# Optimization experiments

Measured on AMD Instinct MI355X. Metric: run time of the kernel, lower is better.

The kernel has to match this reference:

```python
import jax, jax.numpy as jnp
import numpy as np

N, D_IN, F = 65536, 512, 256
E = 524288
BATCH, K1 = 32, 200
BN_EPS = 1e-5


def setup_inputs() -> dict:
    key = jax.random.key(0)
    ks = iter(jax.random.split(key, 64))

    def nrm(shape, s=0.05):
        return jax.random.normal(next(ks), shape, jnp.float32) * s

    inp = {
        "feat": jax.random.normal(next(ks), (N, D_IN), jnp.float32),
        "A": jax.random.randint(next(ks), (2, E), 0, N, dtype=jnp.int32),
        "h1id": jax.random.randint(next(ks), (BATCH * K1,), 0, N // BATCH, dtype=jnp.int32),
        "batch": BATCH,
    }
    dims = [(D_IN, F), (F, F), (F, F), (F, F)]
    for i, (di, do) in enumerate(dims, 1):
        inp[f"eps{i}"] = jnp.zeros((), jnp.float32)          # GINConv train_eps, init 0
        inp[f"w{i}a"] = nrm((di, do)); inp[f"b{i}a"] = jnp.zeros((do,), jnp.float32)
        inp[f"w{i}b"] = nrm((do, do)); inp[f"b{i}b"] = jnp.zeros((do,), jnp.float32)
        inp[f"g{i}"] = jnp.ones((do,), jnp.float32)          # BN gamma
        inp[f"be{i}"] = jnp.zeros((do,), jnp.float32)        # BN beta
        inp[f"m{i}"] = nrm((do,))                            # BN running mean
        inp[f"v{i}"] = jax.random.uniform(next(ks), (do,), jnp.float32, 0.5, 1.5)  # BN running var
    inp["wc1"] = nrm((F, F)); inp["bc1"] = jnp.zeros((F,), jnp.float32)
    inp["pa"] = jnp.full((F,), 0.25, jnp.float32)            # PReLU per-channel slope
    inp["wc2"] = nrm((F, 2)); inp["bc2"] = jnp.zeros((2,), jnp.float32)
    return inp


def _gin_conv(x, src, dst, eps, wa, ba, wb, bb, g, be, m, v):
    # sum aggregation over in-edges: aggr[i] = sum_{(j->i)} x[j]
    aggr = jax.ops.segment_sum(x[src], dst, num_segments=N)
    h = (1.0 + eps) * x + aggr
    h = jax.nn.relu(h @ wa + ba) @ wb + bb
    # BatchNorm1d in eval mode (running stats)
    return (h - m) * jax.lax.rsqrt(v + BN_EPS) * g + be


def _forward(feat, A, h1id, batch,
             eps1, w1a, b1a, w1b, b1b, g1, be1, m1, v1,
             eps2, w2a, b2a, w2b, b2b, g2, be2, m2, v2,
             eps3, w3a, b3a, w3b, b3b, g3, be3, m3, v3,
             eps4, w4a, b4a, w4b, b4b, g4, be4, m4, v4,
             wc1, bc1, pa, wc2, bc2):
    src, dst = A[0], A[1]
    h = jax.nn.relu(_gin_conv(feat, src, dst, eps1, w1a, b1a, w1b, b1b, g1, be1, m1, v1))
    h = jax.nn.relu(_gin_conv(h, src, dst, eps2, w2a, b2a, w2b, b2b, g2, be2, m2, v2))
    h = jax.nn.relu(_gin_conv(h, src, dst, eps3, w3a, b3a, w3b, b3b, g3, be3, m3, v3))
    h = _gin_conv(h, src, dst, eps4, w4a, b4a, w4b, b4b, g4, be4, m4, v4)
    score = h.reshape(batch, -1, F)                      # [B, n_per_graph, F]
    idx = h1id.reshape(batch, K1)
    edge_feat = jnp.take_along_axis(score, idx[:, :, None], axis=1)  # [B, K1, F]
    ef = edge_feat.reshape(-1, F)
    hc = ef @ wc1 + bc1
    hc = jnp.where(hc > 0, hc, pa * hc)                  # PReLU(256)
    return hc @ wc2 + bc2                                # [B*K1, 2]


def reference(feat, A, h1id, batch,
              eps1, w1a, b1a, w1b, b1b, g1, be1, m1, v1,
              eps2, w2a, b2a, w2b, b2b, g2, be2, m2, v2,
              eps3, w3a, b3a, w3b, b3b, g3, be3, m3, v3,
              eps4, w4a, b4a, w4b, b4b, g4, be4, m4, v4,
              wc1, bc1, pa, wc2, bc2):
    return _forward(feat, A, h1id, batch,
                    eps1, w1a, b1a, w1b, b1b, g1, be1, m1, v1,
                    eps2, w2a, b2a, w2b, b2b, g2, be2, m2, v2,
                    eps3, w3a, b3a, w3b, b3b, g3, be3, m3, v3,
                    eps4, w4a, b4a, w4b, b4b, g4, be4, m4, v4,
                    wc1, bc1, pa, wc2, bc2)
```

## Files before the change

kernel.cpp:

```cpp
#include <hip/hip_runtime.h>

typedef unsigned short u16;
typedef unsigned int   u32;
typedef __bf16  bf16x8 __attribute__((ext_vector_type(8)));
typedef float   f32x4  __attribute__((ext_vector_type(4)));
typedef u32     u32x4  __attribute__((ext_vector_type(4)));

#define NN 65536
#define NE 524288
#define FD 256

typedef const __attribute__((address_space(1))) void* gas_p;
typedef __attribute__((address_space(3))) void* las_p;
#define GLDS16(g, l) __builtin_amdgcn_global_load_lds((gas_p)(const void*)(g), (las_p)(void*)(l), 16, 0, 0)

__device__ __forceinline__ u16 f2bf(float f){
  u32 u = __float_as_uint(f);
  u += 0x7fffu + ((u >> 16) & 1u);
  return (u16)(u >> 16);
}
__device__ __forceinline__ float bf2f(u32 lo16){
  return __uint_as_float(lo16 << 16);
}
__device__ __forceinline__ void acc8(float* a, uint4 v){
  a[0] += bf2f(v.x & 0xffffu); a[1] += bf2f(v.x >> 16);
  a[2] += bf2f(v.y & 0xffffu); a[3] += bf2f(v.y >> 16);
  a[4] += bf2f(v.z & 0xffffu); a[5] += bf2f(v.z >> 16);
  a[6] += bf2f(v.w & 0xffffu); a[7] += bf2f(v.w >> 16);
}

__global__ __launch_bounds__(256) void prep_k(
    const float* __restrict__ w1a, const float* __restrict__ w1b,
    const float* __restrict__ w2a, const float* __restrict__ w2b,
    const float* __restrict__ w3a, const float* __restrict__ w3b,
    const float* __restrict__ w4a, const float* __restrict__ w4b,
    const float* __restrict__ wc1, u16* __restrict__ wT)
{
  int idx = blockIdx.x * 256 + threadIdx.x;
  const float* src; int base, K, local;
  if (idx < 131072){ src = w1a; base = 0; K = 512; local = idx; }
  else {
    local = idx - 131072;
    int j = local >> 16;
    local &= 65535;
    K = 256;
    base = 131072 + j * 65536;
    switch (j){
      case 0: src = w1b; break;
      case 1: src = w2a; break;
      case 2: src = w2b; break;
      case 3: src = w3a; break;
      case 4: src = w3b; break;
      case 5: src = w4a; break;
      case 6: src = w4b; break;
      default: src = wc1; break;
    }
  }
  int n = local & 255;
  int k = local >> 8;
  wT[base + n * K + k] = f2bf(src[k * 256 + n]);
}

__global__ __launch_bounds__(256) void hist_k(const int* __restrict__ dst, int* __restrict__ deg){
  int e = blockIdx.x * 256 + threadIdx.x;
  atomicAdd(&deg[dst[e]], 1);
}

__global__ __launch_bounds__(1024) void scan_k(const int* __restrict__ deg, int* __restrict__ rs){
  __shared__ int part[1024];
  int t = threadIdx.x;
  int base = t * 64;
  int sum = 0;
  for (int i = 0; i < 64; ++i) sum += deg[base + i];
  part[t] = sum;
  __syncthreads();
  for (int off = 1; off < 1024; off <<= 1){
    int v = 0;
    if (t >= off) v = part[t - off];
    __syncthreads();
    part[t] += v;
    __syncthreads();
  }
  int run = part[t] - sum;
  for (int i = 0; i < 64; ++i){ rs[base + i] = run; run += deg[base + i]; }
  if (t == 1023) rs[65536] = part[1023];
}

__global__ __launch_bounds__(256) void scat_k(
    const int* __restrict__ src, const int* __restrict__ dst,
    const int* __restrict__ rs, int* __restrict__ cursor, int* __restrict__ csr)
{
  int e = blockIdx.x * 256 + threadIdx.x;
  int d = dst[e];
  int pos = atomicAdd(&cursor[d], 1);
  csr[rs[d] + pos] = src[e];
}

template<int AF32, int MODE, int RELU, int K>
__global__ __launch_bounds__(512) void gemm_k(
    const void* __restrict__ Ap, const u16* __restrict__ Bt,
    u16* __restrict__ C,
    const float* __restrict__ p0, const float* __restrict__ p1,
    const float* __restrict__ p2, const float* __restrict__ p3,
    const float* __restrict__ p4)
{
  __shared__ u16 lds[32768];
  u16* As = lds;
  u16* Bs = lds + 8192;
  const int t    = threadIdx.x;
  const int lane = t & 63;
  const int w    = t >> 6;
  const int wm   = w & 1;
  const int wn   = w >> 1;
  const int m0   = blockIdx.x * 128;
  const int mrow = lane & 15;
  const int quad = lane >> 4;

  f32x4 acc[4][4];
  const f32x4 zero = {0.f, 0.f, 0.f, 0.f};
  #pragma unroll
  for (int i = 0; i < 4; ++i)
    #pragma unroll
    for (int j = 0; j < 4; ++j) acc[i][j] = zero;

  const u16* Ab = (const u16*)Ap;
  const float* Af = (const float*)Ap;

  for (int k0 = 0; k0 < K; k0 += 64){
    if (AF32){
      #pragma unroll
      for (int i = 0; i < 2; ++i){
        int p   = i * 512 + t;
        int row = p >> 3;
        const float* s = Af + (size_t)(m0 + row) * K + k0 + (p & 7) * 8;
        float4 x0 = *(const float4*)s;
        float4 x1 = *(const float4*)(s + 4);
        union { u32x4 q; u16 h[8]; } u;
        u.h[0] = f2bf(x0.x); u.h[1] = f2bf(x0.y); u.h[2] = f2bf(x0.z); u.h[3] = f2bf(x0.w);
        u.h[4] = f2bf(x1.x); u.h[5] = f2bf(x1.y); u.h[6] = f2bf(x1.z); u.h[7] = f2bf(x1.w);
        int dst = (p & ~7) | ((p & 7) ^ (row & 7));
        *(u32x4*)&As[dst * 8] = u.q;
      }
    } else {
      #pragma unroll
      for (int i = 0; i < 2; ++i){
        int p   = i * 512 + t;
        int row = p >> 3;
        int ch  = (p & 7) ^ (row & 7);
        GLDS16(Ab + (size_t)(m0 + row) * K + k0 + ch * 8, &As[p * 8]);
      }
    }
    #pragma unroll
    for (int i = 0; i < 4; ++i){
      int p   = i * 512 + t;
      int row = p >> 3;
      int ch  = (p & 7) ^ (row & 7);
      GLDS16(Bt + (size_t)row * K + k0 + ch * 8, &Bs[p * 8]);
    }
    __syncthreads();
    #pragma unroll
    for (int ks = 0; ks < 2; ++ks){
      bf16x8 af[4], bq[4];
      #pragma unroll
      for (int mi = 0; mi < 4; ++mi){
        int r  = wm * 64 + mi * 16 + mrow;
        int ch = (quad + ks * 4) ^ (r & 7);
        af[mi] = *(const bf16x8*)&As[(r * 8 + ch) * 8];
      }
      #pragma unroll
      for (int ni = 0; ni < 4; ++ni){
        int rb = wn * 64 + ni * 16 + mrow;
        int ch = (quad + ks * 4) ^ (rb & 7);
        bq[ni] = *(const bf16x8*)&Bs[(rb * 8 + ch) * 8];
      }
      #pragma unroll
      for (int mi = 0; mi < 4; ++mi)
        #pragma unroll
        for (int ni = 0; ni < 4; ++ni)
          acc[mi][ni] = __builtin_amdgcn_mfma_f32_16x16x32_bf16(af[mi], bq[ni], acc[mi][ni], 0, 0, 0);
    }
    __syncthreads();
  }

  #pragma unroll
  for (int ni = 0; ni < 4; ++ni){
    int c  = wn * 64 + ni * 16 + mrow;
    float scale = 1.f, shift = 0.f, slope = 0.f;
    if (MODE == 1){
      float s = p0[c] * rsqrtf(p3[c] + 1e-5f);
      scale = s;
      shift = (p4[c] - p2[c]) * s + p1[c];
    }
    if (MODE == 2){ shift = p0[c]; slope = p1[c]; }
    #pragma unroll
    for (int mi = 0; mi < 4; ++mi){
      int rbase = wm * 64 + mi * 16 + quad * 4;
      #pragma unroll
      for (int reg = 0; reg < 4; ++reg){
        float v = acc[mi][ni][reg];
        if (MODE == 1){
          v = v * scale + shift;
          if (RELU) v = fmaxf(v, 0.f);
        }
        if (MODE == 2){
          v += shift;
          v = v > 0.f ? v : slope * v;
        }
        lds[(rbase + reg) * 256 + c] = f2bf(v);
      }
    }
  }
  __syncthreads();
  #pragma unroll
  for (int i = 0; i < 8; ++i){
    int p  = i * 512 + t;
    int r  = p >> 5;
    int ch = p & 31;
    u32x4 q = *(const u32x4*)&lds[r * 256 + ch * 8];
    *(u32x4*)&C[(size_t)(m0 + r) * 256 + ch * 8] = q;
  }
}

template<int GATH>
__global__ __launch_bounds__(256) void agg_k(
    const u16* __restrict__ y, const int* __restrict__ rs, const int* __restrict__ csr,
    const float* __restrict__ epsp, const float* __restrict__ bias,
    const int* __restrict__ gidx, u16* __restrict__ tout)
{
  int sub    = threadIdx.x >> 5;
  int lane32 = threadIdx.x & 31;
  int idx    = blockIdx.x * 8 + sub;
  int node;
  if (GATH) node = (idx / 200) * 2048 + gidx[idx];
  else      node = idx;
  int f0 = lane32 * 8;
  float e1 = 1.0f + epsp[0];
  int s0 = rs[node], s1 = rs[node + 1];
  float a[8] = {0.f,0.f,0.f,0.f,0.f,0.f,0.f,0.f};
  int e = s0;
  for (; e + 4 <= s1; e += 4){
    int sa = csr[e], sb = csr[e+1], sc = csr[e+2], sd = csr[e+3];
    uint4 va = *(const uint4*)(y + (size_t)sa * 256 + f0);
    uint4 vb = *(const uint4*)(y + (size_t)sb * 256 + f0);
    uint4 vc = *(const uint4*)(y + (size_t)sc * 256 + f0);
    uint4 vd = *(const uint4*)(y + (size_t)sd * 256 + f0);
    acc8(a, va); acc8(a, vb); acc8(a, vc); acc8(a, vd);
  }
  for (; e < s1; ++e){
    int s = csr[e];
    acc8(a, *(const uint4*)(y + (size_t)s * 256 + f0));
  }
  uint4 own = *(const uint4*)(y + (size_t)node * 256 + f0);
  float ow[8];
  ow[0] = bf2f(own.x & 0xffffu); ow[1] = bf2f(own.x >> 16);
  ow[2] = bf2f(own.y & 0xffffu); ow[3] = bf2f(own.y >> 16);
  ow[4] = bf2f(own.z & 0xffffu); ow[5] = bf2f(own.z >> 16);
  ow[6] = bf2f(own.w & 0xffffu); ow[7] = bf2f(own.w >> 16);
  float4 b0 = *(const float4*)(bias + f0);
  float4 b1 = *(const float4*)(bias + f0 + 4);
  float r[8];
  r[0] = fmaxf(e1 * ow[0] + a[0] + b0.x, 0.f);
  r[1] = fmaxf(e1 * ow[1] + a[1] + b0.y, 0.f);
  r[2] = fmaxf(e1 * ow[2] + a[2] + b0.z, 0.f);
  r[3] = fmaxf(e1 * ow[3] + a[3] + b0.w, 0.f);
  r[4] = fmaxf(e1 * ow[4] + a[4] + b1.x, 0.f);
  r[5] = fmaxf(e1 * ow[5] + a[5] + b1.y, 0.f);
  r[6] = fmaxf(e1 * ow[6] + a[6] + b1.z, 0.f);
  r[7] = fmaxf(e1 * ow[7] + a[7] + b1.w, 0.f);
  uint4 o;
  o.x = (u32)f2bf(r[0]) | ((u32)f2bf(r[1]) << 16);
  o.y = (u32)f2bf(r[2]) | ((u32)f2bf(r[3]) << 16);
  o.z = (u32)f2bf(r[4]) | ((u32)f2bf(r[5]) << 16);
  o.w = (u32)f2bf(r[6]) | ((u32)f2bf(r[7]) << 16);
  *(uint4*)(tout + (size_t)idx * 256 + f0) = o;
}

__global__ __launch_bounds__(256) void head_k(
    const u16* __restrict__ hc, const float* __restrict__ wc2,
    const float* __restrict__ bc2, float* __restrict__ out)
{
  int row  = blockIdx.x * 4 + (threadIdx.x >> 6);
  int lane = threadIdx.x & 63;
  int f0   = lane * 4;
  uint2 hv = *(const uint2*)(hc + (size_t)row * 256 + f0);
  float h0 = bf2f(hv.x & 0xffffu), h1 = bf2f(hv.x >> 16);
  float h2 = bf2f(hv.y & 0xffffu), h3 = bf2f(hv.y >> 16);
  float4 wa = *(const float4*)(wc2 + f0 * 2);
  float4 wb = *(const float4*)(wc2 + f0 * 2 + 4);
  float acc0 = h0 * wa.x + h1 * wa.z + h2 * wb.x + h3 * wb.z;
  float acc1 = h0 * wa.y + h1 * wa.w + h2 * wb.y + h3 * wb.w;
  #pragma unroll
  for (int off = 32; off > 0; off >>= 1){
    acc0 += __shfl_xor(acc0, off);
    acc1 += __shfl_xor(acc1, off);
  }
  if (lane == 0){
    out[row * 2]     = acc0 + bc2[0];
    out[row * 2 + 1] = acc1 + bc2[1];
  }
}

extern "C" void kernel_launch(void* const* d_in, const int* in_sizes, int n_in,
                              void* d_out, int out_size, void* d_ws, size_t ws_size,
                              hipStream_t stream)
{
  const float* feat = (const float*)d_in[0];
  const int*   A    = (const int*)d_in[1];
  const int*   h1id = (const int*)d_in[2];
  const float* eps[4] = {(const float*)d_in[4],  (const float*)d_in[13], (const float*)d_in[22], (const float*)d_in[31]};
  const float* wa [4] = {(const float*)d_in[5],  (const float*)d_in[14], (const float*)d_in[23], (const float*)d_in[32]};
  const float* ba [4] = {(const float*)d_in[6],  (const float*)d_in[15], (const float*)d_in[24], (const float*)d_in[33]};
  const float* wb [4] = {(const float*)d_in[7],  (const float*)d_in[16], (const float*)d_in[25], (const float*)d_in[34]};
  const float* bb [4] = {(const float*)d_in[8],  (const float*)d_in[17], (const float*)d_in[26], (const float*)d_in[35]};
  const float* g  [4] = {(const float*)d_in[9],  (const float*)d_in[18], (const float*)d_in[27], (const float*)d_in[36]};
  const float* be [4] = {(const float*)d_in[10], (const float*)d_in[19], (const float*)d_in[28], (const float*)d_in[37]};
  const float* m  [4] = {(const float*)d_in[11], (const float*)d_in[20], (const float*)d_in[29], (const float*)d_in[38]};
  const float* v  [4] = {(const float*)d_in[12], (const float*)d_in[21], (const float*)d_in[30], (const float*)d_in[39]};
  const float* wc1 = (const float*)d_in[40];
  const float* bc1 = (const float*)d_in[41];
  const float* pa  = (const float*)d_in[42];
  const float* wc2 = (const float*)d_in[43];
  const float* bc2 = (const float*)d_in[44];

  char* ws = (char*)d_ws;
  u16* wT     = (u16*)(ws + 0);
  int* deg    = (int*)(ws + 1310720);
  int* rs     = (int*)(ws + 1572864);
  int* cursor = (int*)(ws + 1835264);
  int* csr    = (int*)(ws + 2097408);
  u16* ybuf   = (u16*)(ws + 4194560);
  u16* tbuf   = (u16*)(ws + 37748992);
  u16* hbuf   = (u16*)(ws + 71303424);
  u16* h4     = (u16*)(ws + 104857856);
  u16* hc     = (u16*)(ws + 108134656);

  u16* w1aT = wT;
  u16* w1bT = wT + 131072;
  u16* w2aT = wT + 196608;
  u16* w2bT = wT + 262144;
  u16* w3aT = wT + 327680;
  u16* w3bT = wT + 393216;
  u16* w4aT = wT + 458752;
  u16* w4bT = wT + 524288;
  u16* wc1T = wT + 589824;

  hipMemsetAsync(deg, 0, 65536 * 4, stream);
  hipMemsetAsync(cursor, 0, 65536 * 4, stream);
  prep_k<<<2560, 256, 0, stream>>>(wa[0], wb[0], wa[1], wb[1], wa[2], wb[2], wa[3], wb[3], wc1, wT);
  hist_k<<<NE / 256, 256, 0, stream>>>(A + NE, deg);
  scan_k<<<1, 1024, 0, stream>>>(deg, rs);
  scat_k<<<NE / 256, 256, 0, stream>>>(A, A + NE, rs, cursor, csr);

  const u16* waT[4] = {w1aT, w2aT, w3aT, w4aT};
  const u16* wbT[4] = {w1bT, w2bT, w3bT, w4bT};

  gemm_k<1,0,0,512><<<512, 512, 0, stream>>>(feat, waT[0], ybuf,
      nullptr, nullptr, nullptr, nullptr, nullptr);
  agg_k<0><<<NN / 8, 256, 0, stream>>>(ybuf, rs, csr, eps[0], ba[0], nullptr, tbuf);
  gemm_k<0,1,1,256><<<512, 512, 0, stream>>>(tbuf, wbT[0], hbuf,
      g[0], be[0], m[0], v[0], bb[0]);

  for (int l = 1; l <= 2; ++l){
    gemm_k<0,0,0,256><<<512, 512, 0, stream>>>(hbuf, waT[l], ybuf,
        nullptr, nullptr, nullptr, nullptr, nullptr);
    agg_k<0><<<NN / 8, 256, 0, stream>>>(ybuf, rs, csr, eps[l], ba[l], nullptr, tbuf);
    gemm_k<0,1,1,256><<<512, 512, 0, stream>>>(tbuf, wbT[l], hbuf,
        g[l], be[l], m[l], v[l], bb[l]);
  }

  gemm_k<0,0,0,256><<<512, 512, 0, stream>>>(hbuf, waT[3], ybuf,
      nullptr, nullptr, nullptr, nullptr, nullptr);
  agg_k<1><<<800, 256, 0, stream>>>(ybuf, rs, csr, eps[3], ba[3], h1id, tbuf);
  gemm_k<0,1,0,256><<<50, 512, 0, stream>>>(tbuf, wbT[3], h4,
      g[3], be[3], m[3], v[3], bb[3]);

  gemm_k<0,2,0,256><<<50, 512, 0, stream>>>(h4, wc1T, hc,
      bc1, pa, nullptr, nullptr, nullptr);
  head_k<<<1600, 256, 0, stream>>>(hc, wc2, bc2, (float*)d_out);

  (void)in_sizes; (void)n_in; (void)out_size; (void)ws_size;
}
```

Before: 628.6 us.

## Double-buffer GEMM LDS staging with smaller tiles and pre-convert features to bf16

The GEMM kernel now uses 64-row tiles, 256 threads and K-steps of 32. It double-buffers the A and B tiles in LDS, issuing the next global_load_lds batch before computing the current one and using explicit vmcnt waits and barriers. Input features are converted to bf16 by a separate conv_k kernel, so the first GEMM no longer converts fp32 inline. The smaller tiles double the grid size, which raises occupancy, but each B tile is now reloaded by twice as many blocks and the conversion adds an extra pass over the feature matrix.

```diff
diff --git a/kernel.cpp b/kernel.cpp
--- a/kernel.cpp
+++ b/kernel.cpp
@@ -14,6 +14,10 @@
 typedef __attribute__((address_space(3))) void* las_p;
 #define GLDS16(g, l) __builtin_amdgcn_global_load_lds((gas_p)(const void*)(g), (las_p)(void*)(l), 16, 0, 0)
 
+#define PIPE_BARRIER()  asm volatile("s_barrier" ::: "memory")
+#define PIPE_WAIT5()    asm volatile("s_waitcnt vmcnt(5)" ::: "memory")
+#define PIPE_WAIT0()    asm volatile("s_waitcnt vmcnt(0)" ::: "memory")
+
 __device__ __forceinline__ u16 f2bf(float f){
   u32 u = __float_as_uint(f);
   u += 0x7fffu + ((u >> 16) & 1u);
@@ -27,6 +31,16 @@
   a[2] += bf2f(v.y & 0xffffu); a[3] += bf2f(v.y >> 16);
   a[4] += bf2f(v.z & 0xffffu); a[5] += bf2f(v.z >> 16);
   a[6] += bf2f(v.w & 0xffffu); a[7] += bf2f(v.w >> 16);
+}
+
+__global__ __launch_bounds__(256) void conv_k(const float* __restrict__ src, u16* __restrict__ dst){
+  int idx = blockIdx.x * 256 + threadIdx.x;
+  const float4* s = (const float4*)(src + (size_t)idx * 8);
+  float4 x0 = s[0], x1 = s[1];
+  union { u32x4 q; u16 h[8]; } u;
+  u.h[0] = f2bf(x0.x); u.h[1] = f2bf(x0.y); u.h[2] = f2bf(x0.z); u.h[3] = f2bf(x0.w);
+  u.h[4] = f2bf(x1.x); u.h[5] = f2bf(x1.y); u.h[6] = f2bf(x1.z); u.h[7] = f2bf(x1.w);
+  *(u32x4*)(dst + (size_t)idx * 8) = u.q;
 }
 
 __global__ __launch_bounds__(256) void prep_k(
@@ -96,25 +110,22 @@
   csr[rs[d] + pos] = src[e];
 }
 
-template<int AF32, int MODE, int RELU, int K>
-__global__ __launch_bounds__(512) void gemm_k(
-    const void* __restrict__ Ap, const u16* __restrict__ Bt,
+template<int MODE, int RELU, int K>
+__global__ __launch_bounds__(256) void gemm_k(
+    const u16* __restrict__ Ab, const u16* __restrict__ Bt,
     u16* __restrict__ C,
     const float* __restrict__ p0, const float* __restrict__ p1,
     const float* __restrict__ p2, const float* __restrict__ p3,
     const float* __restrict__ p4)
 {
-  __shared__ u16 lds[32768];
-  u16* As = lds;
-  u16* Bs = lds + 8192;
+  __shared__ u16 lds[20480];
   const int t    = threadIdx.x;
   const int lane = t & 63;
-  const int w    = t >> 6;
-  const int wm   = w & 1;
-  const int wn   = w >> 1;
-  const int m0   = blockIdx.x * 128;
+  const int wv   = t >> 6;
+  const int m0   = blockIdx.x * 64;
   const int mrow = lane & 15;
   const int quad = lane >> 4;
+  const int NI   = K / 32;
 
   f32x4 acc[4][4];
   const f32x4 zero = {0.f, 0.f, 0.f, 0.f};
@@ -123,55 +134,47 @@
     #pragma unroll
     for (int j = 0; j < 4; ++j) acc[i][j] = zero;
 
-  const u16* Ab = (const u16*)Ap;
-  const float* Af = (const float*)Ap;
-
-  for (int k0 = 0; k0 < K; k0 += 64){
-    if (AF32){
-      #pragma unroll
-      for (int i = 0; i < 2; ++i){
-        int p   = i * 512 + t;
-        int row = p >> 3;
-        const float* s = Af + (size_t)(m0 + row) * K + k0 + (p & 7) * 8;
-        float4 x0 = *(const float4*)s;
-        float4 x1 = *(const float4*)(s + 4);
-        union { u32x4 q; u16 h[8]; } u;
-        u.h[0] = f2bf(x0.x); u.h[1] = f2bf(x0.y); u.h[2] = f2bf(x0.z); u.h[3] = f2bf(x0.w);
-        u.h[4] = f2bf(x1.x); u.h[5] = f2bf(x1.y); u.h[6] = f2bf(x1.z); u.h[7] = f2bf(x1.w);
-        int dst = (p & ~7) | ((p & 7) ^ (row & 7));
-        *(u32x4*)&As[dst * 8] = u.q;
-      }
-    } else {
-      #pragma unroll
-      for (int i = 0; i < 2; ++i){
-        int p   = i * 512 + t;
-        int row = p >> 3;
-        int ch  = (p & 7) ^ (row & 7);
-        GLDS16(Ab + (size_t)(m0 + row) * K + k0 + ch * 8, &As[p * 8]);
-      }
+  auto stage = [&](int buf, int k0){
+    u16* Asb = lds + (buf ? 2048 : 0);
+    u16* Bsb = lds + (buf ? 12288 : 4096);
+    {
+      int p = t;
+      int row = p >> 2;
+      int ch  = (p & 3) ^ (row & 3);
+      GLDS16(Ab + (size_t)(m0 + row) * K + k0 + ch * 8, &Asb[p * 8]);
     }
     #pragma unroll
     for (int i = 0; i < 4; ++i){
-      int p   = i * 512 + t;
-      int row = p >> 3;
-      int ch  = (p & 7) ^ (row & 7);
-      GLDS16(Bt + (size_t)row * K + k0 + ch * 8, &Bs[p * 8]);
-    }
-    __syncthreads();
-    #pragma unroll
-    for (int ks = 0; ks < 2; ++ks){
+      int q = i * 256 + t;
+      int row = q >> 2;
+      int ch  = (q & 3) ^ (row & 3);
+      GLDS16(Bt + (size_t)row * K + k0 + ch * 8, &Bsb[q * 8]);
+    }
+  };
+
+  stage(0, 0);
+  for (int it = 0; it < NI; ++it){
+    int cur = it & 1;
+    if (it + 1 < NI){
+      stage(cur ^ 1, (it + 1) * 32);
+      PIPE_WAIT5();
+    } else {
+      PIPE_WAIT0();
+    }
+    PIPE_BARRIER();
+    {
+      const u16* As = lds + (cur ? 2048 : 0);
+      const u16* Bs = lds + (cur ? 12288 : 4096);
       bf16x8 af[4], bq[4];
       #pragma unroll
       for (int mi = 0; mi < 4; ++mi){
-        int r  = wm * 64 + mi * 16 + mrow;
-        int ch = (quad + ks * 4) ^ (r & 7);
-        af[mi] = *(const bf16x8*)&As[(r * 8 + ch) * 8];
+        int r = mi * 16 + mrow;
+        af[mi] = *(const bf16x8*)&As[(r * 4 + (quad ^ (r & 3))) * 8];
       }
       #pragma unroll
       for (int ni = 0; ni < 4; ++ni){
-        int rb = wn * 64 + ni * 16 + mrow;
-        int ch = (quad + ks * 4) ^ (rb & 7);
-        bq[ni] = *(const bf16x8*)&Bs[(rb * 8 + ch) * 8];
+        int rb = wv * 64 + ni * 16 + mrow;
+        bq[ni] = *(const bf16x8*)&Bs[(rb * 4 + (quad ^ (rb & 3))) * 8];
       }
       #pragma unroll
       for (int mi = 0; mi < 4; ++mi)
@@ -179,12 +182,12 @@
         for (int ni = 0; ni < 4; ++ni)
           acc[mi][ni] = __builtin_amdgcn_mfma_f32_16x16x32_bf16(af[mi], bq[ni], acc[mi][ni], 0, 0, 0);
     }
-    __syncthreads();
+    PIPE_BARRIER();
   }
 
   #pragma unroll
   for (int ni = 0; ni < 4; ++ni){
-    int c  = wn * 64 + ni * 16 + mrow;
+    int c = wv * 64 + ni * 16 + mrow;
     float scale = 1.f, shift = 0.f, slope = 0.f;
     if (MODE == 1){
       float s = p0[c] * rsqrtf(p3[c] + 1e-5f);
@@ -194,7 +197,7 @@
     if (MODE == 2){ shift = p0[c]; slope = p1[c]; }
     #pragma unroll
     for (int mi = 0; mi < 4; ++mi){
-      int rbase = wm * 64 + mi * 16 + quad * 4;
+      int rbase = mi * 16 + quad * 4;
       #pragma unroll
       for (int reg = 0; reg < 4; ++reg){
         float v = acc[mi][ni][reg];
@@ -213,7 +216,7 @@
   __syncthreads();
   #pragma unroll
   for (int i = 0; i < 8; ++i){
-    int p  = i * 512 + t;
+    int p  = i * 256 + t;
     int r  = p >> 5;
     int ch = p & 31;
     u32x4 q = *(const u32x4*)&lds[r * 256 + ch * 8];
@@ -333,6 +336,7 @@
   u16* hbuf   = (u16*)(ws + 71303424);
   u16* h4     = (u16*)(ws + 104857856);
   u16* hc     = (u16*)(ws + 108134656);
+  u16* featb  = (u16*)(ws + 117440512);
 
   u16* w1aT = wT;
   u16* w1bT = wT + 131072;
@@ -346,6 +350,7 @@
 
   hipMemsetAsync(deg, 0, 65536 * 4, stream);
   hipMemsetAsync(cursor, 0, 65536 * 4, stream);
+  conv_k<<<16384, 256, 0, stream>>>(feat, featb);
   prep_k<<<2560, 256, 0, stream>>>(wa[0], wb[0], wa[1], wb[1], wa[2], wb[2], wa[3], wb[3], wc1, wT);
   hist_k<<<NE / 256, 256, 0, stream>>>(A + NE, deg);
   scan_k<<<1, 1024, 0, stream>>>(deg, rs);
@@ -354,27 +359,27 @@
   const u16* waT[4] = {w1aT, w2aT, w3aT, w4aT};
   const u16* wbT[4] = {w1bT, w2bT, w3bT, w4bT};
 
-  gemm_k<1,0,0,512><<<512, 512, 0, stream>>>(feat, waT[0], ybuf,
+  gemm_k<0,0,512><<<1024, 256, 0, stream>>>(featb, waT[0], ybuf,
       nullptr, nullptr, nullptr, nullptr, nullptr);
   agg_k<0><<<NN / 8, 256, 0, stream>>>(ybuf, rs, csr, eps[0], ba[0], nullptr, tbuf);
-  gemm_k<0,1,1,256><<<512, 512, 0, stream>>>(tbuf, wbT[0], hbuf,
+  gemm_k<1,1,256><<<1024, 256, 0, stream>>>(tbuf, wbT[0], hbuf,
       g[0], be[0], m[0], v[0], bb[0]);
 
   for (int l = 1; l <= 2; ++l){
-    gemm_k<0,0,0,256><<<512, 512, 0, stream>>>(hbuf, waT[l], ybuf,
+    gemm_k<0,0,256><<<1024, 256, 0, stream>>>(hbuf, waT[l], ybuf,
         nullptr, nullptr, nullptr, nullptr, nullptr);
     agg_k<0><<<NN / 8, 256, 0, stream>>>(ybuf, rs, csr, eps[l], ba[l], nullptr, tbuf);
-    gemm_k<0,1,1,256><<<512, 512, 0, stream>>>(tbuf, wbT[l], hbuf,
+    gemm_k<1,1,256><<<1024, 256, 0, stream>>>(tbuf, wbT[l], hbuf,
         g[l], be[l], m[l], v[l], bb[l]);
   }
 
-  gemm_k<0,0,0,256><<<512, 512, 0, stream>>>(hbuf, waT[3], ybuf,
+  gemm_k<0,0,256><<<1024, 256, 0, stream>>>(hbuf, waT[3], ybuf,
       nullptr, nullptr, nullptr, nullptr, nullptr);
   agg_k<1><<<800, 256, 0, stream>>>(ybuf, rs, csr, eps[3], ba[3], h1id, tbuf);
-  gemm_k<0,1,0,256><<<50, 512, 0, stream>>>(tbuf, wbT[3], h4,
+  gemm_k<1,0,256><<<100, 256, 0, stream>>>(tbuf, wbT[3], h4,
       g[3], be[3], m[3], v[3], bb[3]);
 
-  gemm_k<0,2,0,256><<<50, 512, 0, stream>>>(h4, wc1T, hc,
+  gemm_k<2,0,256><<<100, 256, 0, stream>>>(h4, wc1T, hc,
       bc1, pa, nullptr, nullptr, nullptr);
   head_k<<<1600, 256, 0, stream>>>(hc, wc2, bc2, (float*)d_out);
 
```

Measured after the change: 661.7 us. 5.3% more time.

## Fuse aggregation, second MLP GEMM, BN and next layer's first GEMM into one kernel

Applied to the files above, without the earlier changes.

Replaces the per-layer agg_k, gemm_k (Wb+BN) and next-layer gemm_k (Wa) with a single fused kernel. Each block aggregates 64 nodes into LDS, multiplies by Wb with the BN+ReLU epilogue, then multiplies by the next layer's Wa, and writes only the result. This removes two full 65536x256 bf16 round-trips through global memory and two launches per layer. In exchange, B operands are read directly from global without LDS staging, and each block does serial gathers for 8 rows per warp-half, which may lower occupancy and latency hiding.

```diff
diff --git a/kernel.cpp b/kernel.cpp
--- a/kernel.cpp
+++ b/kernel.cpp
@@ -96,13 +96,10 @@
   csr[rs[d] + pos] = src[e];
 }
 
-template<int AF32, int MODE, int RELU, int K>
-__global__ __launch_bounds__(512) void gemm_k(
-    const void* __restrict__ Ap, const u16* __restrict__ Bt,
-    u16* __restrict__ C,
-    const float* __restrict__ p0, const float* __restrict__ p1,
-    const float* __restrict__ p2, const float* __restrict__ p3,
-    const float* __restrict__ p4)
+template<int K>
+__global__ __launch_bounds__(512) void gemm512_k(
+    const float* __restrict__ Af, const u16* __restrict__ Bt,
+    u16* __restrict__ C)
 {
   __shared__ u16 lds[32768];
   u16* As = lds;
@@ -123,32 +120,19 @@
     #pragma unroll
     for (int j = 0; j < 4; ++j) acc[i][j] = zero;
 
-  const u16* Ab = (const u16*)Ap;
-  const float* Af = (const float*)Ap;
-
   for (int k0 = 0; k0 < K; k0 += 64){
-    if (AF32){
-      #pragma unroll
-      for (int i = 0; i < 2; ++i){
-        int p   = i * 512 + t;
-        int row = p >> 3;
-        const float* s = Af + (size_t)(m0 + row) * K + k0 + (p & 7) * 8;
-        float4 x0 = *(const float4*)s;
-        float4 x1 = *(const float4*)(s + 4);
-        union { u32x4 q; u16 h[8]; } u;
-        u.h[0] = f2bf(x0.x); u.h[1] = f2bf(x0.y); u.h[2] = f2bf(x0.z); u.h[3] = f2bf(x0.w);
-        u.h[4] = f2bf(x1.x); u.h[5] = f2bf(x1.y); u.h[6] = f2bf(x1.z); u.h[7] = f2bf(x1.w);
-        int dst = (p & ~7) | ((p & 7) ^ (row & 7));
-        *(u32x4*)&As[dst * 8] = u.q;
-      }
-    } else {
-      #pragma unroll
-      for (int i = 0; i < 2; ++i){
-        int p   = i * 512 + t;
-        int row = p >> 3;
-        int ch  = (p & 7) ^ (row & 7);
-        GLDS16(Ab + (size_t)(m0 + row) * K + k0 + ch * 8, &As[p * 8]);
-      }
+    #pragma unroll
+    for (int i = 0; i < 2; ++i){
+      int p   = i * 512 + t;
+      int row = p >> 3;
+      const float* s = Af + (size_t)(m0 + row) * K + k0 + (p & 7) * 8;
+      float4 x0 = *(const float4*)s;
+      float4 x1 = *(const float4*)(s + 4);
+      union { u32x4 q; u16 h[8]; } u;
+      u.h[0] = f2bf(x0.x); u.h[1] = f2bf(x0.y); u.h[2] = f2bf(x0.z); u.h[3] = f2bf(x0.w);
+      u.h[4] = f2bf(x1.x); u.h[5] = f2bf(x1.y); u.h[6] = f2bf(x1.z); u.h[7] = f2bf(x1.w);
+      int dst = (p & ~7) | ((p & 7) ^ (row & 7));
+      *(u32x4*)&As[dst * 8] = u.q;
     }
     #pragma unroll
     for (int i = 0; i < 4; ++i){
@@ -184,30 +168,13 @@
 
   #pragma unroll
   for (int ni = 0; ni < 4; ++ni){
-    int c  = wn * 64 + ni * 16 + mrow;
-    float scale = 1.f, shift = 0.f, slope = 0.f;
-    if (MODE == 1){
-      float s = p0[c] * rsqrtf(p3[c] + 1e-5f);
-      scale = s;
-      shift = (p4[c] - p2[c]) * s + p1[c];
-    }
-    if (MODE == 2){ shift = p0[c]; slope = p1[c]; }
+    int c = wn * 64 + ni * 16 + mrow;
     #pragma unroll
     for (int mi = 0; mi < 4; ++mi){
       int rbase = wm * 64 + mi * 16 + quad * 4;
       #pragma unroll
-      for (int reg = 0; reg < 4; ++reg){
-        float v = acc[mi][ni][reg];
-        if (MODE == 1){
-          v = v * scale + shift;
-          if (RELU) v = fmaxf(v, 0.f);
-        }
-        if (MODE == 2){
-          v += shift;
-          v = v > 0.f ? v : slope * v;
-        }
-        lds[(rbase + reg) * 256 + c] = f2bf(v);
-      }
+      for (int reg = 0; reg < 4; ++reg)
+        lds[(rbase + reg) * 256 + c] = f2bf(acc[mi][ni][reg]);
     }
   }
   __syncthreads();
@@ -221,58 +188,172 @@
   }
 }
 
-template<int GATH>
-__global__ __launch_bounds__(256) void agg_k(
-    const u16* __restrict__ y, const int* __restrict__ rs, const int* __restrict__ csr,
-    const float* __restrict__ epsp, const float* __restrict__ bias,
-    const int* __restrict__ gidx, u16* __restrict__ tout)
-{
-  int sub    = threadIdx.x >> 5;
-  int lane32 = threadIdx.x & 31;
-  int idx    = blockIdx.x * 8 + sub;
-  int node;
-  if (GATH) node = (idx / 200) * 2048 + gidx[idx];
-  else      node = idx;
-  int f0 = lane32 * 8;
-  float e1 = 1.0f + epsp[0];
-  int s0 = rs[node], s1 = rs[node + 1];
-  float a[8] = {0.f,0.f,0.f,0.f,0.f,0.f,0.f,0.f};
-  int e = s0;
-  for (; e + 4 <= s1; e += 4){
-    int sa = csr[e], sb = csr[e+1], sc = csr[e+2], sd = csr[e+3];
-    uint4 va = *(const uint4*)(y + (size_t)sa * 256 + f0);
-    uint4 vb = *(const uint4*)(y + (size_t)sb * 256 + f0);
-    uint4 vc = *(const uint4*)(y + (size_t)sc * 256 + f0);
-    uint4 vd = *(const uint4*)(y + (size_t)sd * 256 + f0);
-    acc8(a, va); acc8(a, vb); acc8(a, vc); acc8(a, vd);
-  }
-  for (; e < s1; ++e){
-    int s = csr[e];
-    acc8(a, *(const uint4*)(y + (size_t)s * 256 + f0));
-  }
-  uint4 own = *(const uint4*)(y + (size_t)node * 256 + f0);
-  float ow[8];
-  ow[0] = bf2f(own.x & 0xffffu); ow[1] = bf2f(own.x >> 16);
-  ow[2] = bf2f(own.y & 0xffffu); ow[3] = bf2f(own.y >> 16);
-  ow[4] = bf2f(own.z & 0xffffu); ow[5] = bf2f(own.z >> 16);
-  ow[6] = bf2f(own.w & 0xffffu); ow[7] = bf2f(own.w >> 16);
-  float4 b0 = *(const float4*)(bias + f0);
-  float4 b1 = *(const float4*)(bias + f0 + 4);
-  float r[8];
-  r[0] = fmaxf(e1 * ow[0] + a[0] + b0.x, 0.f);
-  r[1] = fmaxf(e1 * ow[1] + a[1] + b0.y, 0.f);
-  r[2] = fmaxf(e1 * ow[2] + a[2] + b0.z, 0.f);
-  r[3] = fmaxf(e1 * ow[3] + a[3] + b0.w, 0.f);
-  r[4] = fmaxf(e1 * ow[4] + a[4] + b1.x, 0.f);
-  r[5] = fmaxf(e1 * ow[5] + a[5] + b1.y, 0.f);
-  r[6] = fmaxf(e1 * ow[6] + a[6] + b1.z, 0.f);
-  r[7] = fmaxf(e1 * ow[7] + a[7] + b1.w, 0.f);
-  uint4 o;
-  o.x = (u32)f2bf(r[0]) | ((u32)f2bf(r[1]) << 16);
-  o.y = (u32)f2bf(r[2]) | ((u32)f2bf(r[3]) << 16);
-  o.z = (u32)f2bf(r[4]) | ((u32)f2bf(r[5]) << 16);
-  o.w = (u32)f2bf(r[6]) | ((u32)f2bf(r[7]) << 16);
-  *(uint4*)(tout + (size_t)idx * 256 + f0) = o;
+template<int GATH, int RELU1, int MODE2>
+__global__ __launch_bounds__(256) void fused_k(
+    const u16* __restrict__ y,
+    const int* __restrict__ rs, const int* __restrict__ csr,
+    const float* __restrict__ epsp, const float* __restrict__ ba,
+    const u16* __restrict__ WbT,
+    const float* __restrict__ g, const float* __restrict__ be,
+    const float* __restrict__ bm, const float* __restrict__ bv,
+    const float* __restrict__ bb,
+    const u16* __restrict__ W2T,
+    const float* __restrict__ q0, const float* __restrict__ q1,
+    const int* __restrict__ gidx,
+    u16* __restrict__ out)
+{
+  __shared__ u16 T[16384];
+  const int t    = threadIdx.x;
+  const int lane = t & 63;
+  const int wv   = t >> 6;
+  const int m0   = blockIdx.x * 64;
+  const int mrow = lane & 15;
+  const int quad = lane >> 4;
+
+  {
+    int sub = t >> 5, lane32 = t & 31;
+    int f0 = lane32 * 8;
+    float e1 = 1.0f + epsp[0];
+    float4 b0 = *(const float4*)(ba + f0);
+    float4 b1 = *(const float4*)(ba + f0 + 4);
+    for (int rr = 0; rr < 8; ++rr){
+      int row = sub * 8 + rr;
+      int idx = m0 + row;
+      int node = GATH ? (idx / 200) * 2048 + gidx[idx] : idx;
+      int s0 = rs[node], s1 = rs[node + 1];
+      float a[8] = {0.f,0.f,0.f,0.f,0.f,0.f,0.f,0.f};
+      int e = s0;
+      for (; e + 4 <= s1; e += 4){
+        int sa = csr[e], sb = csr[e+1], sc = csr[e+2], sd = csr[e+3];
+        uint4 va = *(const uint4*)(y + (size_t)sa * 256 + f0);
+        uint4 vb = *(const uint4*)(y + (size_t)sb * 256 + f0);
+        uint4 vc = *(const uint4*)(y + (size_t)sc * 256 + f0);
+        uint4 vd = *(const uint4*)(y + (size_t)sd * 256 + f0);
+        acc8(a, va); acc8(a, vb); acc8(a, vc); acc8(a, vd);
+      }
+      for (; e < s1; ++e)
+        acc8(a, *(const uint4*)(y + (size_t)csr[e] * 256 + f0));
+      uint4 own = *(const uint4*)(y + (size_t)node * 256 + f0);
+      float r0 = fmaxf(e1 * bf2f(own.x & 0xffffu) + a[0] + b0.x, 0.f);
+      float r1 = fmaxf(e1 * bf2f(own.x >> 16)     + a[1] + b0.y, 0.f);
+      float r2 = fmaxf(e1 * bf2f(own.y & 0xffffu) + a[2] + b0.z, 0.f);
+      float r3 = fmaxf(e1 * bf2f(own.y >> 16)     + a[3] + b0.w, 0.f);
+      float r4 = fmaxf(e1 * bf2f(own.z & 0xffffu) + a[4] + b1.x, 0.f);
+      float r5 = fmaxf(e1 * bf2f(own.z >> 16)     + a[5] + b1.y, 0.f);
+      float r6 = fmaxf(e1 * bf2f(own.w & 0xffffu) + a[6] + b1.z, 0.f);
+      float r7 = fmaxf(e1 * bf2f(own.w >> 16)     + a[7] + b1.w, 0.f);
+      u32x4 o;
+      o.x = (u32)f2bf(r0) | ((u32)f2bf(r1) << 16);
+      o.y = (u32)f2bf(r2) | ((u32)f2bf(r3) << 16);
+      o.z = (u32)f2bf(r4) | ((u32)f2bf(r5) << 16);
+      o.w = (u32)f2bf(r6) | ((u32)f2bf(r7) << 16);
+      int pos = row * 32 + (lane32 ^ (row & 7));
+      *(u32x4*)&T[pos * 8] = o;
+    }
+  }
+  __syncthreads();
+
+  f32x4 acc[4][4];
+  const f32x4 zero = {0.f, 0.f, 0.f, 0.f};
+  #pragma unroll
+  for (int i = 0; i < 4; ++i)
+    #pragma unroll
+    for (int j = 0; j < 4; ++j) acc[i][j] = zero;
+
+  #pragma unroll
+  for (int ks = 0; ks < 8; ++ks){
+    bf16x8 af[4], bq[4];
+    #pragma unroll
+    for (int mi = 0; mi < 4; ++mi){
+      int r  = mi * 16 + mrow;
+      int kc = (ks * 4 + quad) ^ (r & 7);
+      af[mi] = *(const bf16x8*)&T[(r * 32 + kc) * 8];
+    }
+    #pragma unroll
+    for (int ni = 0; ni < 4; ++ni)
+      bq[ni] = *(const bf16x8*)(WbT + (size_t)(wv * 64 + ni * 16 + mrow) * 256 + ks * 32 + quad * 8);
+    #pragma unroll
+    for (int mi = 0; mi < 4; ++mi)
+      #pragma unroll
+      for (int ni = 0; ni < 4; ++ni)
+        acc[mi][ni] = __builtin_amdgcn_mfma_f32_16x16x32_bf16(af[mi], bq[ni], acc[mi][ni], 0, 0, 0);
+  }
+  __syncthreads();
+
+  #pragma unroll
+  for (int ni = 0; ni < 4; ++ni){
+    int c = wv * 64 + ni * 16 + mrow;
+    float s  = g[c] * rsqrtf(bv[c] + 1e-5f);
+    float sh = (bb[c] - bm[c]) * s + be[c];
+    int kc = c >> 3, lo = c & 7;
+    #pragma unroll
+    for (int mi = 0; mi < 4; ++mi){
+      int rb = mi * 16 + quad * 4;
+      #pragma unroll
+      for (int reg = 0; reg < 4; ++reg){
+        int r = rb + reg;
+        float val = acc[mi][ni][reg] * s + sh;
+        if (RELU1) val = fmaxf(val, 0.f);
+        T[(r * 32 + (kc ^ (r & 7))) * 8 + lo] = f2bf(val);
+      }
+    }
+  }
+  __syncthreads();
+
+  #pragma unroll
+  for (int i = 0; i < 4; ++i)
+    #pragma unroll
+    for (int j = 0; j < 4; ++j) acc[i][j] = zero;
+  #pragma unroll
+  for (int ks = 0; ks < 8; ++ks){
+    bf16x8 af[4], bq[4];
+    #pragma unroll
+    for (int mi = 0; mi < 4; ++mi){
+      int r  = mi * 16 + mrow;
+      int kc = (ks * 4 + quad) ^ (r & 7);
+      af[mi] = *(const bf16x8*)&T[(r * 32 + kc) * 8];
+    }
+    #pragma unroll
+    for (int ni = 0; ni < 4; ++ni)
+      bq[ni] = *(const bf16x8*)(W2T + (size_t)(wv * 64 + ni * 16 + mrow) * 256 + ks * 32 + quad * 8);
+    #pragma unroll
+    for (int mi = 0; mi < 4; ++mi)
+      #pragma unroll
+      for (int ni = 0; ni < 4; ++ni)
+        acc[mi][ni] = __builtin_amdgcn_mfma_f32_16x16x32_bf16(af[mi], bq[ni], acc[mi][ni], 0, 0, 0);
+  }
+  __syncthreads();
+
+  #pragma unroll
+  for (int ni = 0; ni < 4; ++ni){
+    int c = wv * 64 + ni * 16 + mrow;
+    float sh = 0.f, sl = 0.f;
+    if (MODE2 == 2){ sh = q0[c]; sl = q1[c]; }
+    int kc = c >> 3, lo = c & 7;
+    #pragma unroll
+    for (int mi = 0; mi < 4; ++mi){
+      int rb = mi * 16 + quad * 4;
+      #pragma unroll
+      for (int reg = 0; reg < 4; ++reg){
+        int r = rb + reg;
+        float val = acc[mi][ni][reg];
+        if (MODE2 == 2){
+          val += sh;
+          val = val > 0.f ? val : sl * val;
+        }
+        T[(r * 32 + (kc ^ (r & 7))) * 8 + lo] = f2bf(val);
+      }
+    }
+  }
+  __syncthreads();
+  #pragma unroll
+  for (int i = 0; i < 8; ++i){
+    int p  = i * 256 + t;
+    int r  = p >> 5;
+    int ch = p & 31;
+    u32x4 q = *(const u32x4*)&T[(r * 32 + (ch ^ (r & 7))) * 8];
+    *(u32x4*)&out[(size_t)(m0 + r) * 256 + ch * 8] = q;
+  }
 }
 
 __global__ __launch_bounds__(256) void head_k(
@@ -328,11 +409,9 @@
   int* rs     = (int*)(ws + 1572864);
   int* cursor = (int*)(ws + 1835264);
   int* csr    = (int*)(ws + 2097408);
-  u16* ybuf   = (u16*)(ws + 4194560);
-  u16* tbuf   = (u16*)(ws + 37748992);
-  u16* hbuf   = (u16*)(ws + 71303424);
-  u16* h4     = (u16*)(ws + 104857856);
-  u16* hc     = (u16*)(ws + 108134656);
+  u16* y0     = (u16*)(ws + 4194560);
+  u16* y1     = (u16*)(ws + 37748992);
+  u16* hc     = (u16*)(ws + 71303424);
 
   u16* w1aT = wT;
   u16* w1bT = wT + 131072;
@@ -351,31 +430,18 @@
   scan_k<<<1, 1024, 0, stream>>>(deg, rs);
   scat_k<<<NE / 256, 256, 0, stream>>>(A, A + NE, rs, cursor, csr);
 
-  const u16* waT[4] = {w1aT, w2aT, w3aT, w4aT};
-  const u16* wbT[4] = {w1bT, w2bT, w3bT, w4bT};
-
-  gemm_k<1,0,0,512><<<512, 512, 0, stream>>>(feat, waT[0], ybuf,
-      nullptr, nullptr, nullptr, nullptr, nullptr);
-  agg_k<0><<<NN / 8, 256, 0, stream>>>(ybuf, rs, csr, eps[0], ba[0], nullptr, tbuf);
-  gemm_k<0,1,1,256><<<512, 512, 0, stream>>>(tbuf, wbT[0], hbuf,
-      g[0], be[0], m[0], v[0], bb[0]);
-
-  for (int l = 1; l <= 2; ++l){
-    gemm_k<0,0,0,256><<<512, 512, 0, stream>>>(hbuf, waT[l], ybuf,
-        nullptr, nullptr, nullptr, nullptr, nullptr);
-    agg_k<0><<<NN / 8, 256, 0, stream>>>(ybuf, rs, csr, eps[l], ba[l], nullptr, tbuf);
-    gemm_k<0,1,1,256><<<512, 512, 0, stream>>>(tbuf, wbT[l], hbuf,
-        g[l], be[l], m[l], v[l], bb[l]);
-  }
-
-  gemm_k<0,0,0,256><<<512, 512, 0, stream>>>(hbuf, waT[3], ybuf,
-      nullptr, nullptr, nullptr, nullptr, nullptr);
-  agg_k<1><<<800, 256, 0, stream>>>(ybuf, rs, csr, eps[3], ba[3], h1id, tbuf);
-  gemm_k<0,1,0,256><<<50, 512, 0, stream>>>(tbuf, wbT[3], h4,
-      g[3], be[3], m[3], v[3], bb[3]);
-
-  gemm_k<0,2,0,256><<<50, 512, 0, stream>>>(h4, wc1T, hc,
-      bc1, pa, nullptr, nullptr, nullptr);
+  gemm512_k<512><<<512, 512, 0, stream>>>(feat, w1aT, y0);
+
+  fused_k<0,1,0><<<1024, 256, 0, stream>>>(y0, rs, csr, eps[0], ba[0], w1bT,
+      g[0], be[0], m[0], v[0], bb[0], w2aT, nullptr, nullptr, nullptr, y1);
+  fused_k<0,1,0><<<1024, 256, 0, stream>>>(y1, rs, csr, eps[1], ba[1], w2bT,
+      g[1], be[1], m[1], v[1], bb[1], w3aT, nullptr, nullptr, nullptr, y0);
+  fused_k<0,1,0><<<1024, 256, 0, stream>>>(y0, rs, csr, eps[2], ba[2], w3bT,
+      g[2], be[2], m[2], v[2], bb[2], w4aT, nullptr, nullptr, nullptr, y1);
+
+  fused_k<1,0,2><<<100, 256, 0, stream>>>(y1, rs, csr, eps[3], ba[3], w4bT,
+      g[3], be[3], m[3], v[3], bb[3], wc1T, bc1, pa, h1id, hc);
+
   head_k<<<1600, 256, 0, stream>>>(hc, wc2, bc2, (float*)d_out);
 
   (void)in_sizes; (void)n_in; (void)out_size; (void)ws_size;
```

New measurement: 720.6 us. +14.6%, slower.
